# Kernel optimization log

Measured on AMD Instinct MI355X. Metric: run time of the kernel, lower is better.

## Reference

```python
import jax, jax.numpy as jnp
import numpy as np

DIM = 2048
N_HEADS = 16
Q_LORA = 1536
KV_LORA = 512
NOPE = 128
ROPE = 64
V_HEAD = 128
QK_HEAD = NOPE + ROPE  # 192
B, S = 2, 2048
SCALE = QK_HEAD ** -0.5
EPS = 1e-6


def rmsnorm(x, w):
    return x * jax.lax.rsqrt(jnp.mean(x * x, axis=-1, keepdims=True) + EPS) * w


def apply_rope(x, cos, sin):
    # x: [b, s, h, d]; cos/sin: [s, d//2]; complex multiply on interleaved pairs
    xr = x.reshape(x.shape[:-1] + (-1, 2))
    c = cos[None, :, None, :]
    s = sin[None, :, None, :]
    re = xr[..., 0] * c - xr[..., 1] * s
    im = xr[..., 0] * s + xr[..., 1] * c
    return jnp.stack([re, im], axis=-1).reshape(x.shape)


def setup_inputs() -> dict:
    key = jax.random.key(0)
    ks = jax.random.split(key, 8)
    w = 0.02
    x = jax.random.normal(ks[0], (B, S, DIM), dtype=jnp.float32)
    # rotary tables
    inv_freq = 1.0 / (10000.0 ** (np.arange(0, ROPE, 2, dtype=np.float32) / ROPE))
    ang = np.arange(S, dtype=np.float32)[:, None] * inv_freq[None, :]
    freqs_cos = jnp.asarray(np.cos(ang))
    freqs_sin = jnp.asarray(np.sin(ang))
    # causal mask (upper triangular large-negative)
    mask = jnp.triu(jnp.full((S, S), -1e9, dtype=jnp.float32), k=1)
    return {
        "x": x,
        "freqs_cos": freqs_cos,
        "freqs_sin": freqs_sin,
        "mask": mask,
        "wq_a": w * jax.random.normal(ks[1], (Q_LORA, DIM), dtype=jnp.float32),
        "q_norm_w": jnp.ones((Q_LORA,), dtype=jnp.float32),
        "wq_b": w * jax.random.normal(ks[2], (N_HEADS * QK_HEAD, Q_LORA), dtype=jnp.float32),
        "wkv_a": w * jax.random.normal(ks[3], (KV_LORA + ROPE, DIM), dtype=jnp.float32),
        "kv_norm_w": jnp.ones((KV_LORA,), dtype=jnp.float32),
        "wkv_b": w * jax.random.normal(ks[4], (N_HEADS * (NOPE + V_HEAD), KV_LORA), dtype=jnp.float32),
        "wo": w * jax.random.normal(ks[5], (DIM, N_HEADS * V_HEAD), dtype=jnp.float32),
    }


def reference(x, freqs_cos, freqs_sin, mask, wq_a, q_norm_w, wq_b, wkv_a, kv_norm_w, wkv_b, wo):
    b, s, _ = x.shape
    # q low-rank path
    q = rmsnorm(x @ wq_a.T, q_norm_w) @ wq_b.T
    q = q.reshape(b, s, N_HEADS, QK_HEAD)
    q_nope, q_pe = q[..., :NOPE], q[..., NOPE:]
    q_pe = apply_rope(q_pe, freqs_cos, freqs_sin)
    # kv latent + decoupled rope key
    kv = x @ wkv_a.T
    c, k_pe = kv[..., :KV_LORA], kv[..., KV_LORA:]
    k_pe = apply_rope(k_pe[:, :, None, :], freqs_cos, freqs_sin)[:, :, 0, :]  # [b,t,r]
    # absorption: fold W^UK into q
    wkvb = wkv_b.reshape(N_HEADS, NOPE + V_HEAD, KV_LORA)
    q_abs = jnp.einsum("bshd,hdc->bshc", q_nope, wkvb[:, :NOPE])
    kv_cache = rmsnorm(c, kv_norm_w)  # [b,t,c] (start_pos=0 prefill)
    # scores over latent + rope parts, fp32 softmax
    scores = (jnp.einsum("bshc,btc->bsht", q_abs, kv_cache)
              + jnp.einsum("bshr,btr->bsht", q_pe, k_pe)) * SCALE
    scores = scores + mask[:, None, :]
    p = jax.nn.softmax(scores.astype(jnp.float32), axis=-1)
    # attend in latent space, then project out with W^UV
    o = jnp.einsum("bsht,btc->bshc", p, kv_cache)
    o = jnp.einsum("bshc,hdc->bshd", o, wkvb[:, -V_HEAD:])
    return o.reshape(b, s, N_HEADS * V_HEAD) @ wo.T
```

## Files before the change

kernel.cpp:

```cpp
#include <hip/hip_runtime.h>

typedef __bf16        bf16x8 __attribute__((ext_vector_type(8)));
typedef float         f32x4  __attribute__((ext_vector_type(4)));

typedef unsigned int __attribute__((address_space(1))) as1_u32;
typedef unsigned int __attribute__((address_space(3))) as3_u32;
#define ASYNC16(gp, lp) __builtin_amdgcn_global_load_lds((as1_u32*)(gp), (as3_u32*)(lp), 16, 0, 0)

#define SCALE_F 0.07216878364870323f
#define LOG2E_F 1.4426950408889634f
#define FQ (SCALE_F * LOG2E_F)

static __device__ __forceinline__ unsigned short f2bf(float f) {
  unsigned int u = __builtin_bit_cast(unsigned int, f);
  u += 0x7fff + ((u >> 16) & 1);
  return (unsigned short)(u >> 16);
}
static __device__ __forceinline__ float bf2f(unsigned short s) {
  unsigned int u = ((unsigned int)s) << 16;
  return __builtin_bit_cast(float, u);
}

__global__ __launch_bounds__(256) void k_f2b(const float* __restrict__ in,
                                             unsigned short* __restrict__ out, int n) {
  int stride = gridDim.x * 256;
  for (int i = blockIdx.x * 256 + threadIdx.x; i < n; i += stride) out[i] = f2bf(in[i]);
}

__global__ __launch_bounds__(256) void k_wkvb(const float* __restrict__ wkvb,
                                              unsigned short* __restrict__ w_nt,
                                              unsigned short* __restrict__ w_v) {
  int i = blockIdx.x * 256 + threadIdx.x;
  int h = i >> 16;
  int rem = i & 65535;
  int c = rem >> 7, d = rem & 127;
  w_nt[i] = f2bf(wkvb[((h << 8) + d) * 512 + c]);
  int d2 = rem >> 9, c2 = rem & 511;
  w_v[i] = f2bf(wkvb[((h << 8) + 128 + d2) * 512 + c2]);
}

template <int BF16_OUT>
__global__ __launch_bounds__(256) void k_gemm(
    const unsigned short* __restrict__ A, int lda, long long sA,
    const unsigned short* __restrict__ W, int ldw, long long sW,
    void* __restrict__ Cv, int ldc, long long sC, int K) {
  __shared__ unsigned short lA[128 * 32];
  __shared__ unsigned short lW[128 * 32];
  const int tid = threadIdx.x;
  const int lane = tid & 63;
  const int q4 = lane >> 4, c16 = lane & 15;
  const int wave = tid >> 6;
  const int wr = (wave >> 1) * 64, wc = (wave & 1) * 64;
  const int z = blockIdx.z;
  A += (long long)z * sA;
  W += (long long)z * sW;

  f32x4 acc[4][4];
#pragma unroll
  for (int i = 0; i < 4; i++)
#pragma unroll
    for (int j = 0; j < 4; j++) acc[i][j] = (f32x4)0.0f;

  const int r = tid >> 2;
  const int cc = (tid & 3) * 8;
  const unsigned short* gA0 = A + ((long long)blockIdx.y * 128 + r) * lda + cc;
  const unsigned short* gA1 = gA0 + (long long)64 * lda;
  const unsigned short* gW0 = W + ((long long)blockIdx.x * 128 + r) * ldw + cc;
  const unsigned short* gW1 = gW0 + (long long)64 * ldw;
  unsigned short* pA0 = &lA[r * 32 + cc];
  unsigned short* pA1 = &lA[(64 + r) * 32 + cc];
  unsigned short* pW0 = &lW[r * 32 + cc];
  unsigned short* pW1 = &lW[(64 + r) * 32 + cc];

  for (int k0 = 0; k0 < K; k0 += 32) {
    ASYNC16(gA0 + k0, pA0);
    ASYNC16(gA1 + k0, pA1);
    ASYNC16(gW0 + k0, pW0);
    ASYNC16(gW1 + k0, pW1);
    __syncthreads();
    bf16x8 af[4], wf[4];
#pragma unroll
    for (int mt = 0; mt < 4; mt++)
      af[mt] = *(const bf16x8*)&lA[(wr + mt * 16 + c16) * 32 + q4 * 8];
#pragma unroll
    for (int nt = 0; nt < 4; nt++)
      wf[nt] = *(const bf16x8*)&lW[(wc + nt * 16 + c16) * 32 + q4 * 8];
#pragma unroll
    for (int mt = 0; mt < 4; mt++)
#pragma unroll
      for (int nt = 0; nt < 4; nt++)
        acc[mt][nt] = __builtin_amdgcn_mfma_f32_16x16x32_bf16(af[mt], wf[nt], acc[mt][nt], 0, 0, 0);
    __syncthreads();
  }

  const long long row0 = (long long)blockIdx.y * 128 + wr + q4 * 4;
  const int col0 = blockIdx.x * 128 + wc + c16;
  if (BF16_OUT) {
    unsigned short* C = (unsigned short*)Cv + (long long)z * sC;
#pragma unroll
    for (int mt = 0; mt < 4; mt++)
#pragma unroll
      for (int i = 0; i < 4; i++) {
        long long rr = (row0 + mt * 16 + i) * (long long)ldc + col0;
#pragma unroll
        for (int nt = 0; nt < 4; nt++) C[rr + nt * 16] = f2bf(acc[mt][nt][i]);
      }
  } else {
    float* C = (float*)Cv + (long long)z * sC;
#pragma unroll
    for (int mt = 0; mt < 4; mt++)
#pragma unroll
      for (int i = 0; i < 4; i++) {
        long long rr = (row0 + mt * 16 + i) * (long long)ldc + col0;
#pragma unroll
        for (int nt = 0; nt < 4; nt++) C[rr + nt * 16] = acc[mt][nt][i];
      }
  }
}

__global__ __launch_bounds__(256) void k_rms_q(const float* __restrict__ in,
                                               const float* __restrict__ w,
                                               unsigned short* __restrict__ out) {
  const int row = blockIdx.x;
  const int tid = threadIdx.x;
  const float* x = in + (long long)row * 1536;
  float v[6], ss = 0.f;
#pragma unroll
  for (int i = 0; i < 6; i++) { v[i] = x[tid + i * 256]; ss += v[i] * v[i]; }
#pragma unroll
  for (int d = 1; d < 64; d <<= 1) ss += __shfl_xor(ss, d);
  __shared__ float red[4];
  if ((tid & 63) == 0) red[tid >> 6] = ss;
  __syncthreads();
  float sc = rsqrtf((red[0] + red[1] + red[2] + red[3]) * (1.0f / 1536.0f) + 1e-6f);
#pragma unroll
  for (int i = 0; i < 6; i++)
    out[(long long)row * 1536 + tid + i * 256] = f2bf(v[i] * sc * w[tid + i * 256]);
}

__global__ __launch_bounds__(256) void k_prep_kv(const float* __restrict__ kvf,
                                                 const float* __restrict__ wn,
                                                 const float* __restrict__ fc,
                                                 const float* __restrict__ fs,
                                                 unsigned short* __restrict__ kvk,
                                                 unsigned short* __restrict__ kvt) {
  const int row = blockIdx.x;
  const int tid = threadIdx.x;
  const float* x = kvf + (long long)row * 640;
  float v0 = x[tid], v1 = x[tid + 256];
  float ss = v0 * v0 + v1 * v1;
#pragma unroll
  for (int d = 1; d < 64; d <<= 1) ss += __shfl_xor(ss, d);
  __shared__ float red[4];
  if ((tid & 63) == 0) red[tid >> 6] = ss;
  __syncthreads();
  float sc = rsqrtf((red[0] + red[1] + red[2] + red[3]) * (1.0f / 512.0f) + 1e-6f);
  const int b = row >> 11, t = row & 2047, tt = t >> 5, tl = t & 31;
  float y0 = v0 * sc * wn[tid], y1 = v1 * sc * wn[tid + 256];
  unsigned short* kb = kvk + (long long)(b * 64 + tt) * 18432;
  unsigned short* vb = kvt + (long long)(b * 64 + tt) * 16384;
  const int d0 = tid, d1 = tid + 256;
  kb[((d0 >> 3) * 32 + tl) * 8 + (d0 & 7)] = f2bf(y0);
  kb[((d1 >> 3) * 32 + tl) * 8 + (d1 & 7)] = f2bf(y1);
  vb[((tl >> 3) * 512 + d0) * 8 + (tl & 7)] = f2bf(y0);
  vb[((tl >> 3) * 512 + d1) * 8 + (tl & 7)] = f2bf(y1);
  if (tid < 32) {
    float x0 = x[512 + 2 * tid], x1 = x[513 + 2 * tid];
    float c = fc[t * 32 + tid], s = fs[t * 32 + tid];
    const int e0 = 512 + 2 * tid, e1 = e0 + 1;
    kb[((e0 >> 3) * 32 + tl) * 8 + (e0 & 7)] = f2bf(x0 * c - x1 * s);
    kb[((e1 >> 3) * 32 + tl) * 8 + (e1 & 7)] = f2bf(x0 * s + x1 * c);
  }
}

__global__ __launch_bounds__(256) void k_repack(const unsigned short* __restrict__ q,
                                                const float* __restrict__ fc,
                                                const float* __restrict__ fs,
                                                unsigned short* __restrict__ qnp,
                                                unsigned short* __restrict__ qcat) {
  const int h = blockIdx.y;
  const int row = blockIdx.x * 4 + (threadIdx.x >> 6);
  const int ln = threadIdx.x & 63;
  const unsigned short* src = q + (long long)row * 3072 + h * 192;
  unsigned short* dn = qnp + ((long long)h * 4096 + row) * 128;
  dn[ln] = f2bf(bf2f(src[ln]) * FQ);
  dn[ln + 64] = f2bf(bf2f(src[ln + 64]) * FQ);
  if (ln < 32) {
    const int t = row & 2047;
    float x0 = bf2f(src[128 + 2 * ln]), x1 = bf2f(src[129 + 2 * ln]);
    float c = fc[t * 32 + ln], s = fs[t * 32 + ln];
    unsigned short* dc = qcat + ((long long)h * 4096 + row) * 576 + 512;
    dc[2 * ln] = f2bf((x0 * c - x1 * s) * FQ);
    dc[2 * ln + 1] = f2bf((x0 * s + x1 * c) * FQ);
  }
}

__global__ __launch_bounds__(256, 2) void k_attn(const unsigned short* __restrict__ qcat,
                                                 const unsigned short* __restrict__ kvk,
                                                 const unsigned short* __restrict__ kvt,
                                                 unsigned short* __restrict__ opk) {
  __shared__ __align__(16) unsigned short kt[18432];
  __shared__ __align__(16) unsigned short vt[16384];
  __shared__ __align__(16) unsigned short pl[4][16][40];
  const int tid = threadIdx.x, lane = tid & 63, wave = tid >> 6;
  const int q4 = lane >> 4, c16 = lane & 15;
  const int bx = blockIdx.x, h = blockIdx.y;
  const int b = (bx >> 2) & 1;
  const int pair = (bx & 3) | ((bx >> 3) << 2);
  const unsigned short* kvk_b = kvk + (long long)b * 64 * 18432;
  const unsigned short* kvt_b = kvt + (long long)b * 64 * 16384;

  bf16x8 ones;
#pragma unroll
  for (int i = 0; i < 8; i++) ones[i] = (__bf16)1.0f;

#define STAGE_K(tile) do {                                                                   \
    const unsigned short* kg_ = kvk_b + (long long)(tile) * 18432;                           \
    _Pragma("unroll")                                                                        \
    for (int i_ = 0; i_ < 9; i_++) { int ch_ = i_ * 256 + tid; ASYNC16(kg_ + ch_ * 8, &kt[ch_ * 8]); } \
  } while (0)
#define STAGE_V(tile) do {                                                                   \
    const unsigned short* vg_ = kvt_b + (long long)(tile) * 16384;                           \
    _Pragma("unroll")                                                                        \
    for (int i_ = 0; i_ < 8; i_++) { int ch_ = i_ * 256 + tid; ASYNC16(vg_ + ch_ * 8, &vt[ch_ * 8]); } \
  } while (0)

  for (int seg = 0; seg < 2; seg++) {
    const int qt = seg ? (31 - pair) : pair;
    const int s_wave = qt * 64 + wave * 16;
    const long long qrow = (long long)h * 4096 + b * 2048 + s_wave;

    bf16x8 qf[18];
    {
      const unsigned short* qp = qcat + (qrow + c16) * 576 + q4 * 8;
#pragma unroll
      for (int kc = 0; kc < 18; kc++) qf[kc] = *(const bf16x8*)(qp + kc * 32);
    }
    f32x4 oacc[32];
#pragma unroll
    for (int i = 0; i < 32; i++) oacc[i] = (f32x4)0.f;
    f32x4 lacc = (f32x4)0.f;

    const int nT = (qt + 1) * 2;
    STAGE_K(0);
    STAGE_V(0);
    __syncthreads();

    for (int tt = 0; tt < nT; tt++) {
      const int t0 = tt * 32;

      f32x4 s0 = (f32x4)0.f, s1 = (f32x4)0.f;
#pragma unroll
      for (int kc = 0; kc < 18; kc++) {
        const unsigned short* kp = &kt[((kc * 4 + q4) * 32 + c16) * 8];
        bf16x8 k0 = *(const bf16x8*)kp;
        bf16x8 k1 = *(const bf16x8*)(kp + 128);
        s0 = __builtin_amdgcn_mfma_f32_16x16x32_bf16(qf[kc], k0, s0, 0, 0, 0);
        s1 = __builtin_amdgcn_mfma_f32_16x16x32_bf16(qf[kc], k1, s1, 0, 0, 0);
      }
      __syncthreads();
      if (tt + 1 < nT) STAGE_K(tt + 1);

#pragma unroll
      for (int i = 0; i < 4; i++) {
        int s_g = s_wave + q4 * 4 + i;
        float v0 = (t0 + c16 > s_g) ? -3.0e38f : s0[i];
        float v1 = (t0 + 16 + c16 > s_g) ? -3.0e38f : s1[i];
        pl[wave][q4 * 4 + i][c16] = f2bf(exp2f(v0));
        pl[wave][q4 * 4 + i][16 + c16] = f2bf(exp2f(v1));
      }
      bf16x8 pf = *(const bf16x8*)&pl[wave][c16][q4 * 8];

      lacc = __builtin_amdgcn_mfma_f32_16x16x32_bf16(pf, ones, lacc, 0, 0, 0);
#pragma unroll
      for (int ct = 0; ct < 32; ct++) {
        bf16x8 vv = *(const bf16x8*)&vt[(q4 * 512 + ct * 16 + c16) * 8];
        oacc[ct] = __builtin_amdgcn_mfma_f32_16x16x32_bf16(pf, vv, oacc[ct], 0, 0, 0);
      }
      __syncthreads();
      if (tt + 1 < nT) STAGE_V(tt + 1);
    }

    const long long orow = qrow + q4 * 4;
#pragma unroll
    for (int i = 0; i < 4; i++) {
      float inv = 1.0f / lacc[i];
      unsigned short* dst = opk + (orow + i) * 512;
#pragma unroll
      for (int ct = 0; ct < 32; ct++) dst[ct * 16 + c16] = f2bf(oacc[ct][i] * inv);
    }
  }
#undef STAGE_K
#undef STAGE_V
}

extern "C" void kernel_launch(void* const* d_in, const int* in_sizes, int n_in,
                              void* d_out, int out_size, void* d_ws, size_t ws_size,
                              hipStream_t stream) {
  (void)in_sizes; (void)n_in; (void)out_size; (void)ws_size;
  const float* x     = (const float*)d_in[0];
  const float* fc    = (const float*)d_in[1];
  const float* fs    = (const float*)d_in[2];
  const float* wq_a  = (const float*)d_in[4];
  const float* qnw   = (const float*)d_in[5];
  const float* wq_b  = (const float*)d_in[6];
  const float* wkv_a = (const float*)d_in[7];
  const float* kvnw  = (const float*)d_in[8];
  const float* wkv_b = (const float*)d_in[9];
  const float* wo    = (const float*)d_in[10];
  float* out = (float*)d_out;
  char* ws = (char*)d_ws;

  const size_t O_WQA  = 0;
  const size_t O_WQB  = 6291456;
  const size_t O_WKVA = 15728640;
  const size_t O_WNT  = 18350080;
  const size_t O_WV   = 20447232;
  const size_t O_WO   = 22544384;
  const size_t O_RA   = 30932992;
  const size_t O_RB   = 47710208;
  const size_t O_QAN  = 72876032;
  const size_t O_KVF  = 85458944;
  const size_t O_KVK  = 95944704;
  const size_t O_KVT  = 100663296;
  const size_t O_QCAT = 104857600;
  const size_t O_OPK  = 180355072;

  unsigned short* W_QA = (unsigned short*)(ws + O_WQA);
  unsigned short* W_QB = (unsigned short*)(ws + O_WQB);
  unsigned short* W_KVA = (unsigned short*)(ws + O_WKVA);
  unsigned short* W_NT = (unsigned short*)(ws + O_WNT);
  unsigned short* W_V  = (unsigned short*)(ws + O_WV);
  unsigned short* W_O  = (unsigned short*)(ws + O_WO);
  unsigned short* X_B  = (unsigned short*)(ws + O_RA);
  unsigned short* QNP  = (unsigned short*)(ws + O_RA);
  unsigned short* OPC  = (unsigned short*)(ws + O_RA);
  float*          QA_F = (float*)(ws + O_RB);
  unsigned short* QB   = (unsigned short*)(ws + O_RB);
  unsigned short* QAN  = (unsigned short*)(ws + O_QAN);
  float*          KV_F = (float*)(ws + O_KVF);
  unsigned short* KVK  = (unsigned short*)(ws + O_KVK);
  unsigned short* KVT  = (unsigned short*)(ws + O_KVT);
  unsigned short* QCAT = (unsigned short*)(ws + O_QCAT);
  unsigned short* OPK  = (unsigned short*)(ws + O_OPK);

  dim3 blk(256);
  k_f2b<<<dim3(4096), blk, 0, stream>>>(x, X_B, 4096 * 2048);
  k_f2b<<<dim3(1024), blk, 0, stream>>>(wq_a, W_QA, 1536 * 2048);
  k_f2b<<<dim3(1024), blk, 0, stream>>>(wq_b, W_QB, 3072 * 1536);
  k_f2b<<<dim3(1024), blk, 0, stream>>>(wkv_a, W_KVA, 576 * 2048);
  k_f2b<<<dim3(1024), blk, 0, stream>>>(wo, W_O, 2048 * 2048);
  k_wkvb<<<dim3(4096), blk, 0, stream>>>(wkv_b, W_NT, W_V);

  k_gemm<0><<<dim3(12, 32, 1), blk, 0, stream>>>(X_B, 2048, 0, W_QA, 2048, 0, QA_F, 1536, 0, 2048);
  k_gemm<0><<<dim3(5, 32, 1), blk, 0, stream>>>(X_B, 2048, 0, W_KVA, 2048, 0, KV_F, 640, 0, 2048);
  k_rms_q<<<dim3(4096), blk, 0, stream>>>(QA_F, qnw, QAN);
  k_prep_kv<<<dim3(4096), blk, 0, stream>>>(KV_F, kvnw, fc, fs, KVK, KVT);
  k_gemm<1><<<dim3(24, 32, 1), blk, 0, stream>>>(QAN, 1536, 0, W_QB, 1536, 0, QB, 3072, 0, 1536);
  k_repack<<<dim3(1024, 16), blk, 0, stream>>>(QB, fc, fs, QNP, QCAT);
  k_gemm<1><<<dim3(4, 32, 16), blk, 0, stream>>>(QNP, 128, 4096LL * 128, W_NT, 128, 512LL * 128,
                                                 QCAT, 576, 4096LL * 576, 128);
  k_attn<<<dim3(32, 16, 1), blk, 0, stream>>>(QCAT, KVK, KVT, OPK);
  k_gemm<1><<<dim3(1, 32, 16), blk, 0, stream>>>(OPK, 512, 4096LL * 512, W_V, 512, 128LL * 512,
                                                 OPC, 2048, 128, 512);
  k_gemm<0><<<dim3(16, 32, 1), blk, 0, stream>>>(OPC, 2048, 0, W_O, 2048, 0, out, 2048, 0, 2048);
}
```

Before: 692.0 us.

## Split attention over key dim across wave pairs with smaller KV tiles

Halves the KV tile to 16 keys and regroups waves into pairs, where each wave in a pair computes half of the 576-wide QK dot product and the pair exchanges partial scores through shared memory. Each wave then accumulates half of the 512 output columns. The grid grows to 128x16 with 32 query rows per block, and the seg loop that paired a short and a long causal tile in one block is removed. This is meant to cut registers and LDS per block so three blocks fit per CU, and to give more blocks to fill the GPU. The cost is an extra barrier and shared-memory exchange per tile, and the loss of the causal load balancing.

```diff
diff --git a/kernel.cpp b/kernel.cpp
--- a/kernel.cpp
+++ b/kernel.cpp
@@ -155,21 +155,21 @@
   if ((tid & 63) == 0) red[tid >> 6] = ss;
   __syncthreads();
   float sc = rsqrtf((red[0] + red[1] + red[2] + red[3]) * (1.0f / 512.0f) + 1e-6f);
-  const int b = row >> 11, t = row & 2047, tt = t >> 5, tl = t & 31;
+  const int b = row >> 11, t = row & 2047, tt = t >> 4, tl = t & 15;
   float y0 = v0 * sc * wn[tid], y1 = v1 * sc * wn[tid + 256];
-  unsigned short* kb = kvk + (long long)(b * 64 + tt) * 18432;
-  unsigned short* vb = kvt + (long long)(b * 64 + tt) * 16384;
+  unsigned short* kb = kvk + (long long)(b * 128 + tt) * 9216;
+  unsigned short* vb = kvt + (long long)(b * 128 + tt) * 8192;
   const int d0 = tid, d1 = tid + 256;
-  kb[((d0 >> 3) * 32 + tl) * 8 + (d0 & 7)] = f2bf(y0);
-  kb[((d1 >> 3) * 32 + tl) * 8 + (d1 & 7)] = f2bf(y1);
+  kb[((d0 >> 3) * 16 + tl) * 8 + (d0 & 7)] = f2bf(y0);
+  kb[((d1 >> 3) * 16 + tl) * 8 + (d1 & 7)] = f2bf(y1);
   vb[((tl >> 3) * 512 + d0) * 8 + (tl & 7)] = f2bf(y0);
   vb[((tl >> 3) * 512 + d1) * 8 + (tl & 7)] = f2bf(y1);
   if (tid < 32) {
     float x0 = x[512 + 2 * tid], x1 = x[513 + 2 * tid];
     float c = fc[t * 32 + tid], s = fs[t * 32 + tid];
     const int e0 = 512 + 2 * tid, e1 = e0 + 1;
-    kb[((e0 >> 3) * 32 + tl) * 8 + (e0 & 7)] = f2bf(x0 * c - x1 * s);
-    kb[((e1 >> 3) * 32 + tl) * 8 + (e1 & 7)] = f2bf(x0 * s + x1 * c);
+    kb[((e0 >> 3) * 16 + tl) * 8 + (e0 & 7)] = f2bf(x0 * c - x1 * s);
+    kb[((e1 >> 3) * 16 + tl) * 8 + (e1 & 7)] = f2bf(x0 * s + x1 * c);
   }
 }
 
@@ -195,100 +195,103 @@
   }
 }
 
-__global__ __launch_bounds__(256, 2) void k_attn(const unsigned short* __restrict__ qcat,
+__global__ __launch_bounds__(256, 3) void k_attn(const unsigned short* __restrict__ qcat,
                                                  const unsigned short* __restrict__ kvk,
                                                  const unsigned short* __restrict__ kvt,
                                                  unsigned short* __restrict__ opk) {
-  __shared__ __align__(16) unsigned short kt[18432];
-  __shared__ __align__(16) unsigned short vt[16384];
+  __shared__ __align__(16) unsigned short kt[9216];
+  __shared__ __align__(16) unsigned short vt[8192];
   __shared__ __align__(16) unsigned short pl[4][16][40];
+  __shared__ float sx[2][2][16][17];
   const int tid = threadIdx.x, lane = tid & 63, wave = tid >> 6;
   const int q4 = lane >> 4, c16 = lane & 15;
+  const int pr = wave >> 1, w01 = wave & 1;
   const int bx = blockIdx.x, h = blockIdx.y;
   const int b = (bx >> 2) & 1;
-  const int pair = (bx & 3) | ((bx >> 3) << 2);
-  const unsigned short* kvk_b = kvk + (long long)b * 64 * 18432;
-  const unsigned short* kvt_b = kvt + (long long)b * 64 * 16384;
-
-  bf16x8 ones;
-#pragma unroll
-  for (int i = 0; i < 8; i++) ones[i] = (__bf16)1.0f;
+  const int qt = 63 - ((bx & 3) | ((bx >> 3) << 2));
+  const unsigned short* kvk_b = kvk + (long long)b * 128 * 9216;
+  const unsigned short* kvt_b = kvt + (long long)b * 128 * 8192;
+
+  {
+    unsigned short* plz = &pl[0][0][0];
+#pragma unroll
+    for (int i = 0; i < 10; i++) plz[tid * 10 + i] = 0;
+  }
+
+  bf16x8 ones8;
+#pragma unroll
+  for (int i = 0; i < 8; i++) ones8[i] = (__bf16)1.0f;
 
 #define STAGE_K(tile) do {                                                                   \
-    const unsigned short* kg_ = kvk_b + (long long)(tile) * 18432;                           \
+    const unsigned short* kg_ = kvk_b + (long long)(tile) * 9216;                            \
     _Pragma("unroll")                                                                        \
-    for (int i_ = 0; i_ < 9; i_++) { int ch_ = i_ * 256 + tid; ASYNC16(kg_ + ch_ * 8, &kt[ch_ * 8]); } \
+    for (int i_ = 0; i_ < 4; i_++) { int ch_ = i_ * 256 + tid; ASYNC16(kg_ + ch_ * 8, &kt[ch_ * 8]); } \
+    if (tid < 128) { int ch_ = 1024 + tid; ASYNC16(kg_ + ch_ * 8, &kt[ch_ * 8]); }           \
   } while (0)
 #define STAGE_V(tile) do {                                                                   \
-    const unsigned short* vg_ = kvt_b + (long long)(tile) * 16384;                           \
+    const unsigned short* vg_ = kvt_b + (long long)(tile) * 8192;                            \
     _Pragma("unroll")                                                                        \
-    for (int i_ = 0; i_ < 8; i_++) { int ch_ = i_ * 256 + tid; ASYNC16(vg_ + ch_ * 8, &vt[ch_ * 8]); } \
+    for (int i_ = 0; i_ < 4; i_++) { int ch_ = i_ * 256 + tid; ASYNC16(vg_ + ch_ * 8, &vt[ch_ * 8]); } \
   } while (0)
 
-  for (int seg = 0; seg < 2; seg++) {
-    const int qt = seg ? (31 - pair) : pair;
-    const int s_wave = qt * 64 + wave * 16;
-    const long long qrow = (long long)h * 4096 + b * 2048 + s_wave;
-
-    bf16x8 qf[18];
-    {
-      const unsigned short* qp = qcat + (qrow + c16) * 576 + q4 * 8;
-#pragma unroll
-      for (int kc = 0; kc < 18; kc++) qf[kc] = *(const bf16x8*)(qp + kc * 32);
+  const int rbase = qt * 32 + pr * 16;
+  const long long qrow = (long long)h * 4096 + b * 2048 + rbase;
+
+  bf16x8 qf[9];
+  {
+    const unsigned short* qp = qcat + (qrow + c16) * 576 + w01 * 288 + q4 * 8;
+#pragma unroll
+    for (int kc = 0; kc < 9; kc++) qf[kc] = *(const bf16x8*)(qp + kc * 32);
+  }
+  f32x4 oacc[16];
+#pragma unroll
+  for (int i = 0; i < 16; i++) oacc[i] = (f32x4)0.f;
+  f32x4 lacc = (f32x4)0.f;
+
+  const int nT = qt * 2 + 2;
+  STAGE_K(0);
+  STAGE_V(0);
+  __syncthreads();
+
+  for (int tt = 0; tt < nT; tt++) {
+    const int t0 = tt * 16;
+
+    f32x4 s0 = (f32x4)0.f;
+#pragma unroll
+    for (int kc = 0; kc < 9; kc++) {
+      bf16x8 k0 = *(const bf16x8*)&kt[(((w01 * 9 + kc) * 4 + q4) * 16 + c16) * 8];
+      s0 = __builtin_amdgcn_mfma_f32_16x16x32_bf16(qf[kc], k0, s0, 0, 0, 0);
     }
-    f32x4 oacc[32];
-#pragma unroll
-    for (int i = 0; i < 32; i++) oacc[i] = (f32x4)0.f;
-    f32x4 lacc = (f32x4)0.f;
-
-    const int nT = (qt + 1) * 2;
-    STAGE_K(0);
-    STAGE_V(0);
+#pragma unroll
+    for (int i = 0; i < 4; i++) sx[pr][w01][q4 * 4 + i][c16] = s0[i];
     __syncthreads();
-
-    for (int tt = 0; tt < nT; tt++) {
-      const int t0 = tt * 32;
-
-      f32x4 s0 = (f32x4)0.f, s1 = (f32x4)0.f;
-#pragma unroll
-      for (int kc = 0; kc < 18; kc++) {
-        const unsigned short* kp = &kt[((kc * 4 + q4) * 32 + c16) * 8];
-        bf16x8 k0 = *(const bf16x8*)kp;
-        bf16x8 k1 = *(const bf16x8*)(kp + 128);
-        s0 = __builtin_amdgcn_mfma_f32_16x16x32_bf16(qf[kc], k0, s0, 0, 0, 0);
-        s1 = __builtin_amdgcn_mfma_f32_16x16x32_bf16(qf[kc], k1, s1, 0, 0, 0);
-      }
-      __syncthreads();
-      if (tt + 1 < nT) STAGE_K(tt + 1);
-
-#pragma unroll
-      for (int i = 0; i < 4; i++) {
-        int s_g = s_wave + q4 * 4 + i;
-        float v0 = (t0 + c16 > s_g) ? -3.0e38f : s0[i];
-        float v1 = (t0 + 16 + c16 > s_g) ? -3.0e38f : s1[i];
-        pl[wave][q4 * 4 + i][c16] = f2bf(exp2f(v0));
-        pl[wave][q4 * 4 + i][16 + c16] = f2bf(exp2f(v1));
-      }
-      bf16x8 pf = *(const bf16x8*)&pl[wave][c16][q4 * 8];
-
-      lacc = __builtin_amdgcn_mfma_f32_16x16x32_bf16(pf, ones, lacc, 0, 0, 0);
-#pragma unroll
-      for (int ct = 0; ct < 32; ct++) {
-        bf16x8 vv = *(const bf16x8*)&vt[(q4 * 512 + ct * 16 + c16) * 8];
-        oacc[ct] = __builtin_amdgcn_mfma_f32_16x16x32_bf16(pf, vv, oacc[ct], 0, 0, 0);
-      }
-      __syncthreads();
-      if (tt + 1 < nT) STAGE_V(tt + 1);
+    if (tt + 1 < nT) STAGE_K(tt + 1);
+
+#pragma unroll
+    for (int i = 0; i < 4; i++) {
+      float sfull = s0[i] + sx[pr][w01 ^ 1][q4 * 4 + i][c16];
+      int s_g = rbase + q4 * 4 + i;
+      float v0 = (t0 + c16 > s_g) ? -3.0e38f : sfull;
+      pl[wave][q4 * 4 + i][c16] = f2bf(exp2f(v0));
     }
 
-    const long long orow = qrow + q4 * 4;
-#pragma unroll
-    for (int i = 0; i < 4; i++) {
-      float inv = 1.0f / lacc[i];
-      unsigned short* dst = opk + (orow + i) * 512;
-#pragma unroll
-      for (int ct = 0; ct < 32; ct++) dst[ct * 16 + c16] = f2bf(oacc[ct][i] * inv);
+    bf16x8 pf = *(const bf16x8*)&pl[wave][c16][q4 * 8];
+    lacc = __builtin_amdgcn_mfma_f32_16x16x32_bf16(pf, ones8, lacc, 0, 0, 0);
+#pragma unroll
+    for (int ct = 0; ct < 16; ct++) {
+      bf16x8 vv = *(const bf16x8*)&vt[((q4 & 1) * 512 + w01 * 256 + ct * 16 + c16) * 8];
+      oacc[ct] = __builtin_amdgcn_mfma_f32_16x16x32_bf16(pf, vv, oacc[ct], 0, 0, 0);
     }
+    __syncthreads();
+    if (tt + 1 < nT) STAGE_V(tt + 1);
+  }
+
+#pragma unroll
+  for (int i = 0; i < 4; i++) {
+    float inv = 1.0f / lacc[i];
+    unsigned short* dst = opk + (qrow + q4 * 4 + i) * 512 + w01 * 256;
+#pragma unroll
+    for (int ct = 0; ct < 16; ct++) dst[ct * 16 + c16] = f2bf(oacc[ct][i] * inv);
   }
 #undef STAGE_K
 #undef STAGE_V
@@ -360,7 +363,7 @@
   k_repack<<<dim3(1024, 16), blk, 0, stream>>>(QB, fc, fs, QNP, QCAT);
   k_gemm<1><<<dim3(4, 32, 16), blk, 0, stream>>>(QNP, 128, 4096LL * 128, W_NT, 128, 512LL * 128,
                                                  QCAT, 576, 4096LL * 576, 128);
-  k_attn<<<dim3(32, 16, 1), blk, 0, stream>>>(QCAT, KVK, KVT, OPK);
+  k_attn<<<dim3(128, 16, 1), blk, 0, stream>>>(QCAT, KVK, KVT, OPK);
   k_gemm<1><<<dim3(1, 32, 16), blk, 0, stream>>>(OPK, 512, 4096LL * 512, W_V, 512, 128LL * 512,
                                                  OPC, 2048, 128, 512);
   k_gemm<0><<<dim3(16, 32, 1), blk, 0, stream>>>(OPC, 2048, 0, W_O, 2048, 0, out, 2048, 0, 2048);
```

After: 903.1 us. 1.31x slower.
